# Optimization experiments

Hardware: AMD Instinct MI355X
Metric: run time of the kernel (lower is better)

The kernel has to match this reference:

```python
import jax, jax.numpy as jnp
import numpy as np

N = 60000      # nodes in batch (max_num_cg_nodes_in_batch = 80000)
E = 150000     # edges per edge type
T = 4          # primary edge types (doubled by add_backwards_edges -> 8)
D = 64         # hidden / embedding size
V = 10000      # subtoken vocab
S = 5          # max subtokens per node label
TIMESTEPS = [7, 1]


def setup_inputs() -> dict:
    key = jax.random.key(0)
    ks = jax.random.split(key, 12)
    sc = 1.0 / np.sqrt(D)
    return {
        "node_subtokens": jax.random.randint(ks[0], (N, S), 0, V),
        "adjacency_lists": jax.random.randint(ks[1], (T, E, 2), 0, N),
        "embed_table": jax.random.normal(ks[2], (V, D), jnp.float32) * 0.1,
        "proj_W": jax.random.normal(ks[3], (D, D), jnp.float32) * sc,
        "edge_W0": jax.random.normal(ks[4], (2 * T, D, D), jnp.float32) * sc,
        "edge_W1": jax.random.normal(ks[5], (2 * T, D, D), jnp.float32) * sc,
        "gru0_Wx": jax.random.normal(ks[6], (D, 3 * D), jnp.float32) * sc,
        "gru0_Wh": jax.random.normal(ks[7], (D, 3 * D), jnp.float32) * sc,
        "gru0_b": jnp.zeros((3 * D,), jnp.float32),
        "gru1_Wx": jax.random.normal(ks[8], (2 * D, 3 * D), jnp.float32) * sc,
        "gru1_Wh": jax.random.normal(ks[9], (D, 3 * D), jnp.float32) * sc,
        "gru1_b": jnp.zeros((3 * D,), jnp.float32),
    }


def _gru(x, h, Wx, Wh, b):
    gx = x @ Wx + b          # [N, 3D]
    gh = h @ Wh              # [N, 3D]
    xr, xu, xc = jnp.split(gx, 3, axis=-1)
    hr, hu, hc = jnp.split(gh, 3, axis=-1)
    r = jax.nn.sigmoid(xr + hr)
    u = jax.nn.sigmoid(xu + hu)
    c = jnp.tanh(xc + r * hc)
    return u * h + (1.0 - u) * c


def reference(node_subtokens, adjacency_lists, embed_table, proj_W,
              edge_W0, edge_W1, gru0_Wx, gru0_Wh, gru0_b,
              gru1_Wx, gru1_Wh, gru1_b):
    # Effective edge types: forward + backward (add_backwards_edges=True)
    srcs = jnp.concatenate([adjacency_lists[:, :, 0], adjacency_lists[:, :, 1]], 0)  # [2T, E]
    dsts = jnp.concatenate([adjacency_lists[:, :, 1], adjacency_lists[:, :, 0]], 0)  # [2T, E]
    flat_dsts = dsts.reshape(-1)

    def aggregate(h, edge_W):
        gathered = h[srcs]                                 # [2T, E, D] gather
        msgs = jnp.einsum('ted,tdk->tek', gathered, edge_W)  # per-edge-type transform
        m = jax.ops.segment_max(msgs.reshape(-1, D), flat_dsts, num_segments=N)
        # nodes with no incoming edges get -inf from segment_max -> zero them
        return jnp.where(jnp.isfinite(m), m, 0.0)

    # Subtoken embedding: mean-pool subtoken embeddings, project to hidden
    node_emb = embed_table[node_subtokens].mean(axis=1)    # [N, D]
    h_init = node_emb @ proj_W                             # [N, D]

    # Layer 0: 7 timesteps, no residual
    h = h_init
    for _ in range(TIMESTEPS[0]):
        h = _gru(aggregate(h, edge_W0), h, gru0_Wx, gru0_Wh, gru0_b)

    # Layer 1: 1 timestep, residual from layer index 0 (= initial node states)
    for _ in range(TIMESTEPS[1]):
        msg = aggregate(h, edge_W1)
        h = _gru(jnp.concatenate([h_init, msg], axis=-1), h, gru1_Wx, gru1_Wh, gru1_b)

    return h  # [N, D] final node representations
```

## Files before the change

kernel.cpp:

```cpp
#include <hip/hip_runtime.h>

typedef short v8s __attribute__((ext_vector_type(8)));
typedef float v4f __attribute__((ext_vector_type(4)));

__device__ __forceinline__ unsigned short f2bf(float x) {
  unsigned u = __float_as_uint(x);
  u = u + 0x7FFFu + ((u >> 16) & 1u);
  return (unsigned short)(u >> 16);
}
__device__ __forceinline__ float bf2f(unsigned short b) {
  return __uint_as_float(((unsigned)b) << 16);
}
__device__ __forceinline__ float sigmoidf_(float x) {
  return 1.f / (1.f + __expf(-x));
}
__device__ __forceinline__ float tanhf_(float x) {
  x = fminf(fmaxf(x, -20.f), 20.f);
  float e2 = __expf(2.f * x);
  return (e2 - 1.f) / (e2 + 1.f);
}

__device__ __forceinline__ void wprep_one(const float* W, unsigned short* O,
                                          int K, int J, int idx) {
  int nkc = K >> 5, nct = J >> 4;
  int j = idx & 7, lane = (idx >> 3) & 63;
  int rest = idx >> 9;
  int ct = rest % nct; rest /= nct;
  int kc = rest % nkc; rest /= nkc;
  int p = rest & 1, t = rest >> 1;
  int row = kc * 32 + (lane >> 4) * 8 + j;
  int col = ct * 16 + (lane & 15);
  float v = W[(size_t)t * K * J + (size_t)row * J + col];
  unsigned short hi = f2bf(v);
  O[idx] = p ? f2bf(v - bf2f(hi)) : hi;
}

__global__ void k_wprep_all(
    const float* eW0, const float* eW1, const float* projW,
    const float* g0Wx, const float* g0Wh, const float* g1Wx, const float* g1Wh,
    unsigned short* eW0f, unsigned short* eW1f, unsigned short* projf,
    unsigned short* g0xf, unsigned short* g0hf,
    unsigned short* g1xf, unsigned short* g1hf) {
  int rel = blockIdx.x * 256 + threadIdx.x;
  if (rel < 65536) { wprep_one(eW0, eW0f, 64, 64, rel); return; }
  rel -= 65536;
  if (rel < 65536) { wprep_one(eW1, eW1f, 64, 64, rel); return; }
  rel -= 65536;
  if (rel < 8192)  { wprep_one(projW, projf, 64, 64, rel); return; }
  rel -= 8192;
  if (rel < 24576) { wprep_one(g0Wx, g0xf, 64, 192, rel); return; }
  rel -= 24576;
  if (rel < 24576) { wprep_one(g0Wh, g0hf, 64, 192, rel); return; }
  rel -= 24576;
  if (rel < 49152) { wprep_one(g1Wx, g1xf, 128, 192, rel); return; }
  rel -= 49152;
  if (rel < 24576) { wprep_one(g1Wh, g1hf, 64, 192, rel); return; }
}

__global__ __launch_bounds__(256) void k_embed(
    const int* __restrict__ toks, const float* __restrict__ embed,
    unsigned short* __restrict__ eh, unsigned short* __restrict__ el, int N) {
  int w = threadIdx.x >> 6, lane = threadIdx.x & 63;
  int n = blockIdx.x * 4 + w;
  if (n >= N) return;
  float acc = 0.f;
#pragma unroll
  for (int s = 0; s < 5; ++s)
    acc += embed[(size_t)toks[n * 5 + s] * 64 + lane];
  float v = acc * 0.2f;
  unsigned short h = f2bf(v);
  eh[(size_t)n * 64 + lane] = h;
  el[(size_t)n * 64 + lane] = f2bf(v - bf2f(h));
}

__global__ void k_counts(const int* __restrict__ adj, int* __restrict__ counts, int E) {
  int e = blockIdx.x * 256 + threadIdx.x;
  if (e >= E) return;
  int t4 = blockIdx.y;
  int2 ab = *(const int2*)&adj[(size_t)(t4 * E + e) * 2];
  atomicAdd(&counts[ab.y], 1);
  atomicAdd(&counts[ab.x], 1);
}

__global__ __launch_bounds__(1024) void k_scan(const int* __restrict__ counts,
                                               int* __restrict__ offsets,
                                               int* __restrict__ cursor, int n) {
  __shared__ int part[1024];
  int tid = threadIdx.x;
  int chunk = (((n + 1023) >> 10) + 3) & ~3;
  int begin = tid * chunk;
  int end = min(begin + chunk, n);
  int s = 0;
  int i = begin;
  for (; i + 4 <= end; i += 4) {
    int4 v = *(const int4*)&counts[i];
    s += v.x + v.y + v.z + v.w;
  }
  for (; i < end; ++i) s += counts[i];
  part[tid] = s;
  __syncthreads();
  for (int off = 1; off < 1024; off <<= 1) {
    int v = (tid >= off) ? part[tid - off] : 0;
    __syncthreads();
    part[tid] += v;
    __syncthreads();
  }
  int run = part[tid] - s;
  i = begin;
  for (; i + 4 <= end; i += 4) {
    int4 c = *(const int4*)&counts[i];
    int4 o;
    o.x = run; o.y = run + c.x; o.z = o.y + c.y; o.w = o.z + c.z;
    *(int4*)&offsets[i] = o;
    *(int4*)&cursor[i] = o;
    run = o.w + c.w;
  }
  for (; i < end; ++i) {
    offsets[i] = run; cursor[i] = run; run += counts[i];
  }
  if (tid == 1023) offsets[n] = part[1023];
}

__global__ void k_fill(const int* __restrict__ adj, int* __restrict__ cursor,
                       int* __restrict__ entries, int E, int N) {
  int e = blockIdx.x * 256 + threadIdx.x;
  if (e >= E) return;
  int t4 = blockIdx.y;
  int2 ab = *(const int2*)&adj[(size_t)(t4 * E + e) * 2];
  int p1 = atomicAdd(&cursor[ab.y], 1);
  entries[p1] = t4 * N + ab.x;
  int p2 = atomicAdd(&cursor[ab.x], 1);
  entries[p2] = (t4 + 4) * N + ab.y;
}

__global__ __launch_bounds__(256) void k_proj(
    const unsigned short* __restrict__ A0h, const unsigned short* __restrict__ A0l,
    const unsigned short* __restrict__ Wf,
    unsigned short* __restrict__ h_hi, unsigned short* __restrict__ h_lo,
    unsigned short* __restrict__ hinit_b, int N) {
  int tid = threadIdx.x;
  int wv = tid >> 6, lane = tid & 63;
  int lr = lane & 15, lg = lane >> 4;
  int m0 = blockIdx.x * 128 + wv * 32;
  v4f acc[2][4] = {};
#pragma unroll
  for (int kc = 0; kc < 2; ++kc) {
    v8s ah[2], al[2];
#pragma unroll
    for (int mt = 0; mt < 2; ++mt) {
      int row = min(m0 + mt * 16 + lr, N - 1);
      size_t off = (size_t)row * 64 + kc * 32 + lg * 8;
      ah[mt] = *(const v8s*)&A0h[off];
      al[mt] = *(const v8s*)&A0l[off];
    }
#pragma unroll
    for (int ct = 0; ct < 4; ++ct) {
      v8s bh = *(const v8s*)&Wf[((size_t)(kc * 4 + ct)) * 512 + lane * 8];
      v8s bl = *(const v8s*)&Wf[((size_t)((2 + kc) * 4 + ct)) * 512 + lane * 8];
#pragma unroll
      for (int mt = 0; mt < 2; ++mt) {
        acc[mt][ct] = __builtin_amdgcn_mfma_f32_16x16x32_bf16(ah[mt], bh, acc[mt][ct], 0, 0, 0);
        acc[mt][ct] = __builtin_amdgcn_mfma_f32_16x16x32_bf16(al[mt], bh, acc[mt][ct], 0, 0, 0);
        acc[mt][ct] = __builtin_amdgcn_mfma_f32_16x16x32_bf16(ah[mt], bl, acc[mt][ct], 0, 0, 0);
      }
    }
  }
#pragma unroll
  for (int ct = 0; ct < 4; ++ct)
#pragma unroll
    for (int mt = 0; mt < 2; ++mt)
#pragma unroll
      for (int r = 0; r < 4; ++r) {
        int m = m0 + mt * 16 + lg * 4 + r;
        if (m >= N) continue;
        int col = ct * 16 + lr;
        float v = acc[mt][ct][r];
        unsigned short hb = f2bf(v);
        h_hi[(size_t)m * 64 + col] = hb;
        h_lo[(size_t)m * 64 + col] = f2bf(v - bf2f(hb));
        hinit_b[(size_t)m * 64 + col] = hb;
      }
}

__global__ __launch_bounds__(256) void k_mm_t(
    const unsigned short* __restrict__ A0h, const unsigned short* __restrict__ A0l,
    const unsigned short* __restrict__ Wf, unsigned short* __restrict__ C16,
    int N) {
  int tid = threadIdx.x;
  int wv = tid >> 6, lane = tid & 63;
  int lr = lane & 15, lg = lane >> 4;
  int y = blockIdx.y;
  const unsigned short* W0 = Wf + (size_t)y * 8192;
  const unsigned short* W1 = Wf + (size_t)(y + 4) * 8192;
  unsigned short* C0 = C16 + (size_t)y * N * 64;
  unsigned short* C1 = C16 + (size_t)(y + 4) * N * 64;
  int m0 = blockIdx.x * 128 + wv * 32;
  v4f acc0[2][4] = {}, acc1[2][4] = {};
#pragma unroll
  for (int kc = 0; kc < 2; ++kc) {
    v8s ah[2], al[2];
#pragma unroll
    for (int mt = 0; mt < 2; ++mt) {
      int row = min(m0 + mt * 16 + lr, N - 1);
      size_t off = (size_t)row * 64 + kc * 32 + lg * 8;
      ah[mt] = *(const v8s*)&A0h[off];
      al[mt] = *(const v8s*)&A0l[off];
    }
#pragma unroll
    for (int ct = 0; ct < 4; ++ct) {
      v8s bh0 = *(const v8s*)&W0[((size_t)(kc * 4 + ct)) * 512 + lane * 8];
      v8s bl0 = *(const v8s*)&W0[((size_t)((2 + kc) * 4 + ct)) * 512 + lane * 8];
      v8s bh1 = *(const v8s*)&W1[((size_t)(kc * 4 + ct)) * 512 + lane * 8];
      v8s bl1 = *(const v8s*)&W1[((size_t)((2 + kc) * 4 + ct)) * 512 + lane * 8];
#pragma unroll
      for (int mt = 0; mt < 2; ++mt) {
        acc0[mt][ct] = __builtin_amdgcn_mfma_f32_16x16x32_bf16(ah[mt], bh0, acc0[mt][ct], 0, 0, 0);
        acc0[mt][ct] = __builtin_amdgcn_mfma_f32_16x16x32_bf16(al[mt], bh0, acc0[mt][ct], 0, 0, 0);
        acc0[mt][ct] = __builtin_amdgcn_mfma_f32_16x16x32_bf16(ah[mt], bl0, acc0[mt][ct], 0, 0, 0);
        acc1[mt][ct] = __builtin_amdgcn_mfma_f32_16x16x32_bf16(ah[mt], bh1, acc1[mt][ct], 0, 0, 0);
        acc1[mt][ct] = __builtin_amdgcn_mfma_f32_16x16x32_bf16(al[mt], bh1, acc1[mt][ct], 0, 0, 0);
        acc1[mt][ct] = __builtin_amdgcn_mfma_f32_16x16x32_bf16(ah[mt], bl1, acc1[mt][ct], 0, 0, 0);
      }
    }
  }
#pragma unroll
  for (int ct = 0; ct < 4; ++ct)
#pragma unroll
    for (int mt = 0; mt < 2; ++mt)
#pragma unroll
      for (int r = 0; r < 4; ++r) {
        int m = m0 + mt * 16 + lg * 4 + r;
        if (m < N) {
          C0[(size_t)m * 64 + ct * 16 + lr] = f2bf(acc0[mt][ct][r]);
          C1[(size_t)m * 64 + ct * 16 + lr] = f2bf(acc1[mt][ct][r]);
        }
      }
}

__global__ __launch_bounds__(256) void k_aggmax(
    const unsigned short* __restrict__ Htb, const int* __restrict__ offsets,
    const int* __restrict__ entries, unsigned short* __restrict__ mh, int N) {
  int w = threadIdx.x >> 6, lane = threadIdx.x & 63;
  int n = blockIdx.x * 4 + w;
  if (n >= N) return;
  int beg = offsets[n], end = offsets[n + 1];
  int g = lane >> 4, q = lane & 15;
  float a0 = -3.4e38f, a1 = a0, a2 = a0, a3 = a0;
  float b0 = a0, b1 = a0, b2 = a0, b3 = a0;
  int i = beg;
  for (; i + 8 <= end; i += 8) {
    int eA = entries[i + g];
    int eB = entries[i + 4 + g];
    ushort4 va = *(const ushort4*)&Htb[(size_t)eA * 64 + q * 4];
    ushort4 vb = *(const ushort4*)&Htb[(size_t)eB * 64 + q * 4];
    a0 = fmaxf(a0, bf2f(va.x)); a1 = fmaxf(a1, bf2f(va.y));
    a2 = fmaxf(a2, bf2f(va.z)); a3 = fmaxf(a3, bf2f(va.w));
    b0 = fmaxf(b0, bf2f(vb.x)); b1 = fmaxf(b1, bf2f(vb.y));
    b2 = fmaxf(b2, bf2f(vb.z)); b3 = fmaxf(b3, bf2f(vb.w));
  }
  for (; i < end; i += 4) {
    int idx = min(i + g, end - 1);
    int e = entries[idx];
    ushort4 va = *(const ushort4*)&Htb[(size_t)e * 64 + q * 4];
    a0 = fmaxf(a0, bf2f(va.x)); a1 = fmaxf(a1, bf2f(va.y));
    a2 = fmaxf(a2, bf2f(va.z)); a3 = fmaxf(a3, bf2f(va.w));
  }
  a0 = fmaxf(a0, b0); a1 = fmaxf(a1, b1); a2 = fmaxf(a2, b2); a3 = fmaxf(a3, b3);
  a0 = fmaxf(a0, __shfl_xor(a0, 16)); a1 = fmaxf(a1, __shfl_xor(a1, 16));
  a2 = fmaxf(a2, __shfl_xor(a2, 16)); a3 = fmaxf(a3, __shfl_xor(a3, 16));
  a0 = fmaxf(a0, __shfl_xor(a0, 32)); a1 = fmaxf(a1, __shfl_xor(a1, 32));
  a2 = fmaxf(a2, __shfl_xor(a2, 32)); a3 = fmaxf(a3, __shfl_xor(a3, 32));
  if (g == 0) {
    ushort4 o;
    if (end > beg) {
      o.x = f2bf(a0); o.y = f2bf(a1); o.z = f2bf(a2); o.w = f2bf(a3);
    } else {
      o.x = 0; o.y = 0; o.z = 0; o.w = 0;
    }
    *(ushort4*)&mh[(size_t)n * 64 + q * 4] = o;
  }
}

template <int NKCX>
__global__ __launch_bounds__(256) void k_gru(
    const unsigned short* __restrict__ x0, const unsigned short* __restrict__ x1,
    const unsigned short* __restrict__ hh, const unsigned short* __restrict__ hl,
    const unsigned short* __restrict__ Wxf, const unsigned short* __restrict__ Whf,
    const float* __restrict__ bias,
    float* outF, unsigned short* oh, unsigned short* ol, int N) {
  int tid = threadIdx.x;
  int wv = tid >> 6, lane = tid & 63;
  int lr = lane & 15, lg = lane >> 4;
  int m0 = blockIdx.x * 128 + wv * 32;
  v4f acc[2][12] = {};
  v4f acch[2][4] = {};
#pragma unroll
  for (int kc = 0; kc < NKCX; ++kc) {
    const unsigned short* X = (NKCX == 4 && kc >= 2) ? x1 : x0;
    int kcl = kc & 1;
    v8s ax[2];
#pragma unroll
    for (int mt = 0; mt < 2; ++mt) {
      int row = min(m0 + mt * 16 + lr, N - 1);
      ax[mt] = *(const v8s*)&X[(size_t)row * 64 + kcl * 32 + lg * 8];
    }
#pragma unroll
    for (int ct = 0; ct < 12; ++ct) {
      v8s bh = *(const v8s*)&Wxf[((size_t)(kc * 12 + ct)) * 512 + lane * 8];
      v8s bl = *(const v8s*)&Wxf[((size_t)((NKCX + kc) * 12 + ct)) * 512 + lane * 8];
#pragma unroll
      for (int mt = 0; mt < 2; ++mt) {
        acc[mt][ct] = __builtin_amdgcn_mfma_f32_16x16x32_bf16(ax[mt], bh, acc[mt][ct], 0, 0, 0);
        acc[mt][ct] = __builtin_amdgcn_mfma_f32_16x16x32_bf16(ax[mt], bl, acc[mt][ct], 0, 0, 0);
      }
    }
  }
#pragma unroll
  for (int kc = 0; kc < 2; ++kc) {
    v8s ah[2], al[2];
#pragma unroll
    for (int mt = 0; mt < 2; ++mt) {
      int row = min(m0 + mt * 16 + lr, N - 1);
      size_t off = (size_t)row * 64 + kc * 32 + lg * 8;
      ah[mt] = *(const v8s*)&hh[off];
      al[mt] = *(const v8s*)&hl[off];
    }
#pragma unroll
    for (int ct = 0; ct < 12; ++ct) {
      v8s bh = *(const v8s*)&Whf[((size_t)(kc * 12 + ct)) * 512 + lane * 8];
      v8s bl = *(const v8s*)&Whf[((size_t)((2 + kc) * 12 + ct)) * 512 + lane * 8];
#pragma unroll
      for (int mt = 0; mt < 2; ++mt) {
        v4f* d = (ct < 8) ? &acc[mt][ct] : &acch[mt][ct - 8];
        *d = __builtin_amdgcn_mfma_f32_16x16x32_bf16(ah[mt], bh, *d, 0, 0, 0);
        *d = __builtin_amdgcn_mfma_f32_16x16x32_bf16(al[mt], bh, *d, 0, 0, 0);
        *d = __builtin_amdgcn_mfma_f32_16x16x32_bf16(ah[mt], bl, *d, 0, 0, 0);
      }
    }
  }
#pragma unroll
  for (int mt = 0; mt < 2; ++mt)
#pragma unroll
    for (int ctg = 0; ctg < 4; ++ctg)
#pragma unroll
      for (int r = 0; r < 4; ++r) {
        int m = m0 + mt * 16 + lg * 4 + r;
        if (m >= N) continue;
        int col = ctg * 16 + lr;
        float hv = bf2f(hh[(size_t)m * 64 + col]) + bf2f(hl[(size_t)m * 64 + col]);
        float rr = sigmoidf_(acc[mt][ctg][r] + bias[col]);
        float uu = sigmoidf_(acc[mt][ctg + 4][r] + bias[64 + col]);
        float cc = tanhf_(acc[mt][ctg + 8][r] + bias[128 + col] + rr * acch[mt][ctg][r]);
        float ho = uu * hv + (1.f - uu) * cc;
        if (outF) outF[(size_t)m * 64 + col] = ho;
        if (oh) {
          unsigned short hb = f2bf(ho);
          oh[(size_t)m * 64 + col] = hb;
          ol[(size_t)m * 64 + col] = f2bf(ho - bf2f(hb));
        }
      }
}

extern "C" void kernel_launch(void* const* d_in, const int* in_sizes, int n_in,
                              void* d_out, int out_size, void* d_ws, size_t ws_size,
                              hipStream_t stream) {
  const int*   toks  = (const int*)d_in[0];
  const int*   adj   = (const int*)d_in[1];
  const float* embed = (const float*)d_in[2];
  const float* projW = (const float*)d_in[3];
  const float* eW0   = (const float*)d_in[4];
  const float* eW1   = (const float*)d_in[5];
  const float* g0Wx  = (const float*)d_in[6];
  const float* g0Wh  = (const float*)d_in[7];
  const float* g0b   = (const float*)d_in[8];
  const float* g1Wx  = (const float*)d_in[9];
  const float* g1Wh  = (const float*)d_in[10];
  const float* g1b   = (const float*)d_in[11];
  float* out = (float*)d_out;

  int N = in_sizes[0] / 5;
  int E = in_sizes[1] / 8;
  size_t ND = (size_t)N * 64;

  char* p = (char*)d_ws;
  unsigned short* Htb     = (unsigned short*)p; p += 8 * ND * 2;
  unsigned short* h_hi    = (unsigned short*)p; p += ND * 2;
  unsigned short* h_lo    = (unsigned short*)p; p += ND * 2;
  unsigned short* hinit_b = (unsigned short*)p; p += ND * 2;
  unsigned short* m_hi    = (unsigned short*)p; p += ND * 2;
  int* offsets = (int*)p; p += (size_t)(N + 64) * sizeof(int);
  int* cnt_cur = (int*)p; p += (size_t)(N + 64) * sizeof(int);
  int* entries = (int*)p; p += (size_t)8 * E * sizeof(int);
  unsigned short* eW0f  = (unsigned short*)p; p += 65536 * 2;
  unsigned short* eW1f  = (unsigned short*)p; p += 65536 * 2;
  unsigned short* projf = (unsigned short*)p; p += 8192 * 2;
  unsigned short* g0xf  = (unsigned short*)p; p += 24576 * 2;
  unsigned short* g0hf  = (unsigned short*)p; p += 24576 * 2;
  unsigned short* g1xf  = (unsigned short*)p; p += 49152 * 2;
  unsigned short* g1hf  = (unsigned short*)p; p += 24576 * 2;
  if ((size_t)(p - (char*)d_ws) > ws_size) return;

  unsigned short* emb_h = Htb;
  unsigned short* emb_l = Htb + ND;

  int g128 = (N + 127) / 128;
  int g4 = (N + 3) / 4;

  k_wprep_all<<<1024, 256, 0, stream>>>(eW0, eW1, projW, g0Wx, g0Wh, g1Wx, g1Wh,
                                        eW0f, eW1f, projf, g0xf, g0hf, g1xf, g1hf);
  hipMemsetAsync(cnt_cur, 0, (size_t)N * sizeof(int), stream);
  dim3 egrid((E + 255) / 256, 4);
  k_counts<<<egrid, 256, 0, stream>>>(adj, cnt_cur, E);
  k_embed<<<g4, 256, 0, stream>>>(toks, embed, emb_h, emb_l, N);
  k_proj<<<g128, 256, 0, stream>>>(emb_h, emb_l, projf, h_hi, h_lo, hinit_b, N);
  k_scan<<<1, 1024, 0, stream>>>(cnt_cur, offsets, cnt_cur, N);
  k_fill<<<egrid, 256, 0, stream>>>(adj, cnt_cur, entries, E, N);

  for (int it = 0; it < 8; ++it) {
    const unsigned short* ef = (it < 7) ? eW0f : eW1f;
    k_mm_t<<<dim3(g128, 4), 256, 0, stream>>>(h_hi, h_lo, ef, Htb, N);
    k_aggmax<<<g4, 256, 0, stream>>>(Htb, offsets, entries, m_hi, N);
    if (it < 7) {
      k_gru<2><<<g128, 256, 0, stream>>>(m_hi, nullptr, h_hi, h_lo,
                                         g0xf, g0hf, g0b,
                                         nullptr, h_hi, h_lo, N);
    } else {
      k_gru<4><<<g128, 256, 0, stream>>>(hinit_b, m_hi, h_hi, h_lo,
                                         g1xf, g1hf, g1b,
                                         out, nullptr, nullptr, N);
    }
  }
}
```

Before: 1.112 ms.

## Fuse aggregation, GRU and next-step edge transform into one per-iteration kernel

Merges the segment-max aggregation, the GRU update and the next timestep's per-edge-type transform into a single kernel per iteration. Messages and the new hidden state stay in swizzled LDS instead of going through global memory, and the transformed tables are double-buffered across iterations. This cuts launches and global round trips for m_hi and h. In exchange, each wave now aggregates 32 nodes serially, which lowers parallelism in the gather phase, and the higher register and LDS use may reduce occupancy.

```diff
diff --git a/kernel.cpp b/kernel.cpp
--- a/kernel.cpp
+++ b/kernel.cpp
@@ -18,6 +18,9 @@
   x = fminf(fmaxf(x, -20.f), 20.f);
   float e2 = __expf(2.f * x);
   return (e2 - 1.f) / (e2 + 1.f);
+}
+__device__ __forceinline__ int swz(int row, int byteInRow) {
+  return row * 128 + (byteInRow ^ ((row & 7) << 4));
 }
 
 __device__ __forceinline__ void wprep_one(const float* W, unsigned short* O,
@@ -237,72 +240,80 @@
       }
 }
 
-__global__ __launch_bounds__(256) void k_aggmax(
-    const unsigned short* __restrict__ Htb, const int* __restrict__ offsets,
-    const int* __restrict__ entries, unsigned short* __restrict__ mh, int N) {
-  int w = threadIdx.x >> 6, lane = threadIdx.x & 63;
-  int n = blockIdx.x * 4 + w;
-  if (n >= N) return;
-  int beg = offsets[n], end = offsets[n + 1];
-  int g = lane >> 4, q = lane & 15;
-  float a0 = -3.4e38f, a1 = a0, a2 = a0, a3 = a0;
-  float b0 = a0, b1 = a0, b2 = a0, b3 = a0;
-  int i = beg;
-  for (; i + 8 <= end; i += 8) {
-    int eA = entries[i + g];
-    int eB = entries[i + 4 + g];
-    ushort4 va = *(const ushort4*)&Htb[(size_t)eA * 64 + q * 4];
-    ushort4 vb = *(const ushort4*)&Htb[(size_t)eB * 64 + q * 4];
-    a0 = fmaxf(a0, bf2f(va.x)); a1 = fmaxf(a1, bf2f(va.y));
-    a2 = fmaxf(a2, bf2f(va.z)); a3 = fmaxf(a3, bf2f(va.w));
-    b0 = fmaxf(b0, bf2f(vb.x)); b1 = fmaxf(b1, bf2f(vb.y));
-    b2 = fmaxf(b2, bf2f(vb.z)); b3 = fmaxf(b3, bf2f(vb.w));
-  }
-  for (; i < end; i += 4) {
-    int idx = min(i + g, end - 1);
-    int e = entries[idx];
-    ushort4 va = *(const ushort4*)&Htb[(size_t)e * 64 + q * 4];
-    a0 = fmaxf(a0, bf2f(va.x)); a1 = fmaxf(a1, bf2f(va.y));
-    a2 = fmaxf(a2, bf2f(va.z)); a3 = fmaxf(a3, bf2f(va.w));
-  }
-  a0 = fmaxf(a0, b0); a1 = fmaxf(a1, b1); a2 = fmaxf(a2, b2); a3 = fmaxf(a3, b3);
-  a0 = fmaxf(a0, __shfl_xor(a0, 16)); a1 = fmaxf(a1, __shfl_xor(a1, 16));
-  a2 = fmaxf(a2, __shfl_xor(a2, 16)); a3 = fmaxf(a3, __shfl_xor(a3, 16));
-  a0 = fmaxf(a0, __shfl_xor(a0, 32)); a1 = fmaxf(a1, __shfl_xor(a1, 32));
-  a2 = fmaxf(a2, __shfl_xor(a2, 32)); a3 = fmaxf(a3, __shfl_xor(a3, 32));
-  if (g == 0) {
-    ushort4 o;
-    if (end > beg) {
-      o.x = f2bf(a0); o.y = f2bf(a1); o.z = f2bf(a2); o.w = f2bf(a3);
-    } else {
-      o.x = 0; o.y = 0; o.z = 0; o.w = 0;
-    }
-    *(ushort4*)&mh[(size_t)n * 64 + q * 4] = o;
-  }
-}
-
-template <int NKCX>
-__global__ __launch_bounds__(256) void k_gru(
-    const unsigned short* __restrict__ x0, const unsigned short* __restrict__ x1,
-    const unsigned short* __restrict__ hh, const unsigned short* __restrict__ hl,
+template <int FINAL>
+__global__ __launch_bounds__(256) void k_iter(
+    const unsigned short* __restrict__ HtR, const int* __restrict__ offsets,
+    const int* __restrict__ entries,
+    unsigned short* __restrict__ hh, unsigned short* __restrict__ hl,
+    const unsigned short* __restrict__ hinit_b,
     const unsigned short* __restrict__ Wxf, const unsigned short* __restrict__ Whf,
-    const float* __restrict__ bias,
-    float* outF, unsigned short* oh, unsigned short* ol, int N) {
+    const float* __restrict__ bias, const unsigned short* __restrict__ eWf,
+    unsigned short* __restrict__ HtW, float* __restrict__ outF, int N) {
+  __shared__ __align__(16) char lds_msg[128 * 128];
+  __shared__ __align__(16) char lds_hs[FINAL ? 16 : 2 * 128 * 128];
   int tid = threadIdx.x;
   int wv = tid >> 6, lane = tid & 63;
   int lr = lane & 15, lg = lane >> 4;
-  int m0 = blockIdx.x * 128 + wv * 32;
+  int lbase = wv * 32;
+  int m0 = blockIdx.x * 128 + lbase;
+
+  int g = lane >> 4, q = lane & 15;
+  for (int i32 = 0; i32 < 32; ++i32) {
+    int n = min(m0 + i32, N - 1);
+    int beg = offsets[n], end = offsets[n + 1];
+    float a0 = -3.4e38f, a1 = a0, a2 = a0, a3 = a0;
+    float b0 = a0, b1 = a0, b2 = a0, b3 = a0;
+    int i = beg;
+    for (; i + 8 <= end; i += 8) {
+      int eA = entries[i + g];
+      int eB = entries[i + 4 + g];
+      ushort4 va = *(const ushort4*)&HtR[(size_t)eA * 64 + q * 4];
+      ushort4 vb = *(const ushort4*)&HtR[(size_t)eB * 64 + q * 4];
+      a0 = fmaxf(a0, bf2f(va.x)); a1 = fmaxf(a1, bf2f(va.y));
+      a2 = fmaxf(a2, bf2f(va.z)); a3 = fmaxf(a3, bf2f(va.w));
+      b0 = fmaxf(b0, bf2f(vb.x)); b1 = fmaxf(b1, bf2f(vb.y));
+      b2 = fmaxf(b2, bf2f(vb.z)); b3 = fmaxf(b3, bf2f(vb.w));
+    }
+    for (; i < end; i += 4) {
+      int idx = min(i + g, end - 1);
+      int e = entries[idx];
+      ushort4 va = *(const ushort4*)&HtR[(size_t)e * 64 + q * 4];
+      a0 = fmaxf(a0, bf2f(va.x)); a1 = fmaxf(a1, bf2f(va.y));
+      a2 = fmaxf(a2, bf2f(va.z)); a3 = fmaxf(a3, bf2f(va.w));
+    }
+    a0 = fmaxf(a0, b0); a1 = fmaxf(a1, b1); a2 = fmaxf(a2, b2); a3 = fmaxf(a3, b3);
+    a0 = fmaxf(a0, __shfl_xor(a0, 16)); a1 = fmaxf(a1, __shfl_xor(a1, 16));
+    a2 = fmaxf(a2, __shfl_xor(a2, 16)); a3 = fmaxf(a3, __shfl_xor(a3, 16));
+    a0 = fmaxf(a0, __shfl_xor(a0, 32)); a1 = fmaxf(a1, __shfl_xor(a1, 32));
+    a2 = fmaxf(a2, __shfl_xor(a2, 32)); a3 = fmaxf(a3, __shfl_xor(a3, 32));
+    if (g == 0) {
+      ushort4 o;
+      if (end > beg) {
+        o.x = f2bf(a0); o.y = f2bf(a1); o.z = f2bf(a2); o.w = f2bf(a3);
+      } else {
+        o.x = 0; o.y = 0; o.z = 0; o.w = 0;
+      }
+      int row = lbase + i32;
+      *(ushort4*)(lds_msg + swz(row, q * 8)) = o;
+    }
+  }
+
+  const int NKCX = FINAL ? 4 : 2;
   v4f acc[2][12] = {};
   v4f acch[2][4] = {};
 #pragma unroll
   for (int kc = 0; kc < NKCX; ++kc) {
-    const unsigned short* X = (NKCX == 4 && kc >= 2) ? x1 : x0;
     int kcl = kc & 1;
     v8s ax[2];
 #pragma unroll
     for (int mt = 0; mt < 2; ++mt) {
-      int row = min(m0 + mt * 16 + lr, N - 1);
-      ax[mt] = *(const v8s*)&X[(size_t)row * 64 + kcl * 32 + lg * 8];
+      if (FINAL && kc < 2) {
+        int row = min(m0 + mt * 16 + lr, N - 1);
+        ax[mt] = *(const v8s*)&hinit_b[(size_t)row * 64 + kcl * 32 + lg * 8];
+      } else {
+        int row = lbase + mt * 16 + lr;
+        ax[mt] = *(const v8s*)(lds_msg + swz(row, kcl * 64 + lg * 16));
+      }
     }
 #pragma unroll
     for (int ct = 0; ct < 12; ++ct) {
@@ -345,20 +356,78 @@
 #pragma unroll
       for (int r = 0; r < 4; ++r) {
         int m = m0 + mt * 16 + lg * 4 + r;
-        if (m >= N) continue;
         int col = ctg * 16 + lr;
-        float hv = bf2f(hh[(size_t)m * 64 + col]) + bf2f(hl[(size_t)m * 64 + col]);
+        unsigned short hbv = hh[(size_t)min(m, N - 1) * 64 + col];
+        unsigned short hlv = hl[(size_t)min(m, N - 1) * 64 + col];
+        float hv = bf2f(hbv) + bf2f(hlv);
         float rr = sigmoidf_(acc[mt][ctg][r] + bias[col]);
         float uu = sigmoidf_(acc[mt][ctg + 4][r] + bias[64 + col]);
         float cc = tanhf_(acc[mt][ctg + 8][r] + bias[128 + col] + rr * acch[mt][ctg][r]);
         float ho = uu * hv + (1.f - uu) * cc;
-        if (outF) outF[(size_t)m * 64 + col] = ho;
-        if (oh) {
-          unsigned short hb = f2bf(ho);
-          oh[(size_t)m * 64 + col] = hb;
-          ol[(size_t)m * 64 + col] = f2bf(ho - bf2f(hb));
+        if (FINAL) {
+          if (m < N) outF[(size_t)m * 64 + col] = ho;
+        } else {
+          unsigned short ohi = f2bf(ho);
+          unsigned short olo = f2bf(ho - bf2f(ohi));
+          if (m < N) {
+            hh[(size_t)m * 64 + col] = ohi;
+            hl[(size_t)m * 64 + col] = olo;
+          }
+          int row = lbase + mt * 16 + lg * 4 + r;
+          *(unsigned short*)(lds_hs + swz(row, col * 2)) = ohi;
+          *(unsigned short*)(lds_hs + 128 * 128 + swz(row, col * 2)) = olo;
         }
       }
+
+  if (FINAL) return;
+
+  v8s tah[2][2], tal[2][2];
+#pragma unroll
+  for (int kc = 0; kc < 2; ++kc)
+#pragma unroll
+    for (int mt = 0; mt < 2; ++mt) {
+      int row = lbase + mt * 16 + lr;
+      tah[kc][mt] = *(const v8s*)(lds_hs + swz(row, kc * 64 + lg * 16));
+      tal[kc][mt] = *(const v8s*)(lds_hs + 128 * 128 + swz(row, kc * 64 + lg * 16));
+    }
+#pragma unroll
+  for (int y = 0; y < 4; ++y) {
+    const unsigned short* W0 = eWf + (size_t)y * 8192;
+    const unsigned short* W1 = eWf + (size_t)(y + 4) * 8192;
+    unsigned short* C0 = HtW + (size_t)y * N * 64;
+    unsigned short* C1 = HtW + (size_t)(y + 4) * N * 64;
+    v4f acc0[2][4] = {}, acc1[2][4] = {};
+#pragma unroll
+    for (int kc = 0; kc < 2; ++kc)
+#pragma unroll
+      for (int ct = 0; ct < 4; ++ct) {
+        v8s bh0 = *(const v8s*)&W0[((size_t)(kc * 4 + ct)) * 512 + lane * 8];
+        v8s bl0 = *(const v8s*)&W0[((size_t)((2 + kc) * 4 + ct)) * 512 + lane * 8];
+        v8s bh1 = *(const v8s*)&W1[((size_t)(kc * 4 + ct)) * 512 + lane * 8];
+        v8s bl1 = *(const v8s*)&W1[((size_t)((2 + kc) * 4 + ct)) * 512 + lane * 8];
+#pragma unroll
+        for (int mt = 0; mt < 2; ++mt) {
+          acc0[mt][ct] = __builtin_amdgcn_mfma_f32_16x16x32_bf16(tah[kc][mt], bh0, acc0[mt][ct], 0, 0, 0);
+          acc0[mt][ct] = __builtin_amdgcn_mfma_f32_16x16x32_bf16(tal[kc][mt], bh0, acc0[mt][ct], 0, 0, 0);
+          acc0[mt][ct] = __builtin_amdgcn_mfma_f32_16x16x32_bf16(tah[kc][mt], bl0, acc0[mt][ct], 0, 0, 0);
+          acc1[mt][ct] = __builtin_amdgcn_mfma_f32_16x16x32_bf16(tah[kc][mt], bh1, acc1[mt][ct], 0, 0, 0);
+          acc1[mt][ct] = __builtin_amdgcn_mfma_f32_16x16x32_bf16(tal[kc][mt], bh1, acc1[mt][ct], 0, 0, 0);
+          acc1[mt][ct] = __builtin_amdgcn_mfma_f32_16x16x32_bf16(tah[kc][mt], bl1, acc1[mt][ct], 0, 0, 0);
+        }
+      }
+#pragma unroll
+    for (int ct = 0; ct < 4; ++ct)
+#pragma unroll
+      for (int mt = 0; mt < 2; ++mt)
+#pragma unroll
+        for (int r = 0; r < 4; ++r) {
+          int m = m0 + mt * 16 + lg * 4 + r;
+          if (m < N) {
+            C0[(size_t)m * 64 + ct * 16 + lr] = f2bf(acc0[mt][ct][r]);
+            C1[(size_t)m * 64 + ct * 16 + lr] = f2bf(acc1[mt][ct][r]);
+          }
+        }
+  }
 }
 
 extern "C" void kernel_launch(void* const* d_in, const int* in_sizes, int n_in,
@@ -383,11 +452,11 @@
   size_t ND = (size_t)N * 64;
 
   char* p = (char*)d_ws;
-  unsigned short* Htb     = (unsigned short*)p; p += 8 * ND * 2;
+  unsigned short* Ht0     = (unsigned short*)p; p += 8 * ND * 2;
+  unsigned short* Ht1     = (unsigned short*)p; p += 8 * ND * 2;
   unsigned short* h_hi    = (unsigned short*)p; p += ND * 2;
   unsigned short* h_lo    = (unsigned short*)p; p += ND * 2;
   unsigned short* hinit_b = (unsigned short*)p; p += ND * 2;
-  unsigned short* m_hi    = (unsigned short*)p; p += ND * 2;
   int* offsets = (int*)p; p += (size_t)(N + 64) * sizeof(int);
   int* cnt_cur = (int*)p; p += (size_t)(N + 64) * sizeof(int);
   int* entries = (int*)p; p += (size_t)8 * E * sizeof(int);
@@ -400,8 +469,8 @@
   unsigned short* g1hf  = (unsigned short*)p; p += 24576 * 2;
   if ((size_t)(p - (char*)d_ws) > ws_size) return;
 
-  unsigned short* emb_h = Htb;
-  unsigned short* emb_l = Htb + ND;
+  unsigned short* emb_h = Ht0;
+  unsigned short* emb_l = Ht0 + ND;
 
   int g128 = (N + 127) / 128;
   int g4 = (N + 3) / 4;
@@ -415,19 +484,18 @@
   k_proj<<<g128, 256, 0, stream>>>(emb_h, emb_l, projf, h_hi, h_lo, hinit_b, N);
   k_scan<<<1, 1024, 0, stream>>>(cnt_cur, offsets, cnt_cur, N);
   k_fill<<<egrid, 256, 0, stream>>>(adj, cnt_cur, entries, E, N);
-
-  for (int it = 0; it < 8; ++it) {
-    const unsigned short* ef = (it < 7) ? eW0f : eW1f;
-    k_mm_t<<<dim3(g128, 4), 256, 0, stream>>>(h_hi, h_lo, ef, Htb, N);
-    k_aggmax<<<g4, 256, 0, stream>>>(Htb, offsets, entries, m_hi, N);
-    if (it < 7) {
-      k_gru<2><<<g128, 256, 0, stream>>>(m_hi, nullptr, h_hi, h_lo,
-                                         g0xf, g0hf, g0b,
-                                         nullptr, h_hi, h_lo, N);
-    } else {
-      k_gru<4><<<g128, 256, 0, stream>>>(hinit_b, m_hi, h_hi, h_lo,
-                                         g1xf, g1hf, g1b,
-                                         out, nullptr, nullptr, N);
-    }
-  }
-}
+  k_mm_t<<<dim3(g128, 4), 256, 0, stream>>>(h_hi, h_lo, eW0f, Ht0, N);
+
+  unsigned short* bufs[2] = {Ht0, Ht1};
+  for (int it = 0; it < 7; ++it) {
+    unsigned short* HtR = bufs[it & 1];
+    unsigned short* HtW = bufs[(it + 1) & 1];
+    const unsigned short* ef = (it < 6) ? eW0f : eW1f;
+    k_iter<0><<<g128, 256, 0, stream>>>(HtR, offsets, entries, h_hi, h_lo,
+                                        hinit_b, g0xf, g0hf, g0b, ef,
+                                        HtW, nullptr, N);
+  }
+  k_iter<1><<<g128, 256, 0, stream>>>(bufs[1], offsets, entries, h_hi, h_lo,
+                                      hinit_b, g1xf, g1hf, g1b, nullptr,
+                                      nullptr, out, N);
+}
```

New measurement: 1.226 ms. 10.2% more time.
